# Performance work log

Measured on AMD Instinct MI355X. Metric: run time of the kernel, lower is better.

The kernel has to match this reference:

```python
import jax, jax.numpy as jnp
import numpy as np

H, HKV, D, HID = 64, 8, 64, 2880
T = 2048
WINDOW = 128
THETA = 150000.0
FACTOR = 32.0
ORIG_MAX = 4096
BETA_FAST, BETA_SLOW = 32.0, 1.0
EPS = 1e-5
SCALE = D ** -0.5
MSCALE = float(0.1 * np.log(FACTOR) + 1.0)  # vLLM YaRN attention mscale


def _yarn_inv_freq():
    # vLLM YaRNScalingRotaryEmbedding inverse frequencies
    def corr_dim(n_rot):
        return D * np.log(ORIG_MAX / (n_rot * 2.0 * np.pi)) / (2.0 * np.log(THETA))
    low = max(int(np.floor(corr_dim(BETA_FAST))), 0)
    high = min(int(np.ceil(corr_dim(BETA_SLOW))), D - 1)
    pow_ = np.arange(0, D, 2, dtype=np.float32) / D
    extrap = 1.0 / (THETA ** pow_)                 # extrapolation inv_freq
    interp = extrap / FACTOR                        # interpolation inv_freq
    ramp = np.clip((np.arange(D // 2, dtype=np.float32) - low) / max(high - low, 1e-3), 0.0, 1.0)
    extrap_mask = 1.0 - ramp
    inv_freq = interp * (1.0 - extrap_mask) + extrap * extrap_mask
    return jnp.asarray(inv_freq, jnp.float32)

_INV_FREQ = _yarn_inv_freq()


def _rope(positions, x):
    # neox-style rotation; x: [T, heads, D]
    freqs = positions.astype(jnp.float32)[:, None] * _INV_FREQ[None, :]  # [T, D/2]
    cos = (jnp.cos(freqs) * MSCALE)[:, None, :]
    sin = (jnp.sin(freqs) * MSCALE)[:, None, :]
    x1, x2 = x[..., : D // 2], x[..., D // 2 :]
    return jnp.concatenate([x1 * cos - x2 * sin, x2 * cos + x1 * sin], axis=-1)


def _attn(q, k, v, sinks):
    # q: [T,H,D]; k,v: [T,HKV,D]; sinks: [H] extra softmax logit per head
    g = H // HKV
    k = jnp.repeat(k, g, axis=1)
    v = jnp.repeat(v, g, axis=1)
    scores = jnp.einsum('qhd,khd->hqk', q, k) * SCALE  # [H,T,T]
    i = jnp.arange(T)[:, None]
    j = jnp.arange(T)[None, :]
    mask = (j <= i) & (i - j < WINDOW)  # causal + sliding window (even layer)
    scores = jnp.where(mask[None], scores, -jnp.inf)
    s = sinks[:, None]                                    # [H,1]
    m = jnp.maximum(jnp.max(scores, axis=-1), s)          # [H,T]
    p = jnp.exp(scores - m[..., None])                    # [H,T,T]
    denom = jnp.sum(p, axis=-1) + jnp.exp(s - m)          # sink adds to denominator only
    out = jnp.einsum('hqk,khd->qhd', p, v) / denom.T[..., None]
    return out.reshape(T, H * D)


def setup_inputs() -> dict:
    key = jax.random.key(0)
    ks = jax.random.split(key, 8)
    return {
        'hidden_states': jax.random.normal(ks[0], (T, HID), jnp.float32),
        'positions': jnp.arange(T, dtype=jnp.int32),
        'norm_w': jnp.ones((HID,), jnp.float32),
        'w_qkv': jax.random.normal(ks[1], ((H + 2 * HKV) * D, HID), jnp.float32) * 0.02,
        'b_qkv': jax.random.normal(ks[2], ((H + 2 * HKV) * D,), jnp.float32) * 0.02,
        'w_o': jax.random.normal(ks[3], (HID, H * D), jnp.float32) * 0.02,
        'b_o': jax.random.normal(ks[4], (HID,), jnp.float32) * 0.02,
        'sinks': jax.random.normal(ks[5], (H,), jnp.float32),
    }


def reference(hidden_states, positions, norm_w, w_qkv, b_qkv, w_o, b_o, sinks):
    x = hidden_states
    t = x * jax.lax.rsqrt(jnp.mean(x * x, axis=-1, keepdims=True) + EPS) * norm_w  # RMSNorm
    qkv = t @ w_qkv.T + b_qkv
    q, k, v = jnp.split(qkv, [H * D, H * D + HKV * D], axis=-1)
    q = _rope(positions, q.reshape(T, H, D))
    k = _rope(positions, k.reshape(T, HKV, D))
    v = v.reshape(T, HKV, D)
    attn_out = _attn(q, k, v, sinks)
    out = attn_out @ w_o.T + b_o
    return out + x  # residual
```

## Files before the change

kernel.cpp:

```cpp
#include <hip/hip_runtime.h>
#include <hip/hip_bf16.h>
#include <stdint.h>

typedef __attribute__((ext_vector_type(8))) short bf16x8;
typedef __attribute__((ext_vector_type(4))) float f32x4;
typedef __attribute__((ext_vector_type(4))) unsigned short u16x4;

#define T_SEQ 2048
#define HID_D 2880
#define KPAD 2944
#define NH 64
#define NKV 8
#define HD 64
#define QKV_N 5120
#define ATT_N 4096
#define WIN 128
#define RSCALE 0.125f
#define MSCALE 1.3465735903f
#define ROPE_TOT (T_SEQ * (NH + NKV) * 32)
#define VT_TOT (NKV * HD * T_SEQ)

__device__ __forceinline__ unsigned short f2bf(float f) {
  union { float f; unsigned u; } v; v.f = f;
  unsigned r = v.u + 0x7fffu + ((v.u >> 16) & 1u);
  return (unsigned short)(r >> 16);
}
__device__ __forceinline__ float bf2f(unsigned short u) {
  union { unsigned u; float f; } v; v.u = ((unsigned)u) << 16;
  return v.f;
}

__device__ __forceinline__ void gload_lds16(const void* g, void* l) {
  __builtin_amdgcn_global_load_lds((const __attribute__((address_space(1))) char*)g,
                                   (__attribute__((address_space(3))) char*)l, 16, 0, 0);
}

__global__ __launch_bounds__(256) void pre_kernel(const float* __restrict__ x,
                                                  const float* __restrict__ w,
                                                  unsigned short* __restrict__ t_bf,
                                                  const float* __restrict__ wq_src,
                                                  unsigned short* __restrict__ wq_dst) {
  __shared__ float red[256];
  if (blockIdx.x < 2048) {
    int row = blockIdx.x;
    const float4* xr4 = (const float4*)(x + (size_t)row * HID_D);
    const float4* w4 = (const float4*)w;
    float ss = 0.f;
    for (int i = threadIdx.x; i < 720; i += 256) {
      float4 v = xr4[i];
      ss += v.x * v.x + v.y * v.y + v.z * v.z + v.w * v.w;
    }
    red[threadIdx.x] = ss;
    __syncthreads();
    for (int s = 128; s > 0; s >>= 1) {
      if (threadIdx.x < s) red[threadIdx.x] += red[threadIdx.x + s];
      __syncthreads();
    }
    float rs = rsqrtf(red[0] / (float)HID_D + 1e-5f);
    u16x4* ob = (u16x4*)(t_bf + (size_t)row * KPAD);
    for (int i = threadIdx.x; i < 736; i += 256) {
      u16x4 o = {0, 0, 0, 0};
      if (i < 720) {
        float4 v = xr4[i];
        float4 g = w4[i];
        o = { f2bf(v.x * rs * g.x), f2bf(v.y * rs * g.y),
              f2bf(v.z * rs * g.z), f2bf(v.w * rs * g.w) };
      }
      ob[i] = o;
    }
  } else {
    const int total = QKV_N * 736;
    for (int i = (blockIdx.x - 2048) * 256 + threadIdx.x; i < total; i += 1024 * 256) {
      int c4 = i % 736, row = i / 736;
      u16x4 o = {0, 0, 0, 0};
      if (c4 < 720) {
        float4 v = ((const float4*)wq_src)[(size_t)row * 720 + c4];
        o = { f2bf(v.x), f2bf(v.y), f2bf(v.z), f2bf(v.w) };
      }
      ((u16x4*)wq_dst)[i] = o;
    }
  }
}

__device__ __forceinline__ void gemm_body(const unsigned short* __restrict__ A,
                                          const unsigned short* __restrict__ B,
                                          unsigned short* __restrict__ C,
                                          const float* __restrict__ bias,
                                          int N, int ld, int nt,
                                          int nbx, int nstore, int swz,
                                          unsigned short* sA, unsigned short* sB) {
  const int tid = threadIdx.x;
  const int lane = tid & 63, wid = tid >> 6;
  const int wr = wid >> 2, wc = wid & 3;
  const int lq = lane & 15, ro = lane >> 4;

  const int bx = swz % nbx, by = swz / nbx;
  const int m0 = by * 256, n0 = bx * 256;

  const int R0 = tid >> 3;
  const int g0 = (((tid & 7) ^ (R0 & 7)) << 3);
  const size_t aOff = (size_t)(m0 + R0) * ld + g0;
  size_t bOff[2][2];
#pragma unroll
  for (int h = 0; h < 2; ++h)
#pragma unroll
    for (int r = 0; r < 2; ++r) {
      int rr = n0 + h * 128 + r * 64 + R0;
      bOff[h][r] = (size_t)rr * ld + g0;
    }

  const int ck0 = ((ro ^ (lq & 7)) << 3);
  const int ck1 = (((4 + ro) ^ (lq & 7)) << 3);

#define STG_A(BUF, H, KT)                                                        \
  { unsigned short* _d = sA + ((BUF) * 2 + (H)) * 8192 + wid * 512;              \
    const unsigned short* _s = A + aOff + (size_t)((H) * 128) * ld + (KT) * 64;  \
    gload_lds16(_s, _d); gload_lds16(_s + (size_t)64 * ld, _d + 4096); }
#define STG_B(BUF, H, KT)                                                        \
  { unsigned short* _d = sB + ((BUF) * 2 + (H)) * 8192 + wid * 512;              \
    gload_lds16(B + bOff[H][0] + (KT) * 64, _d);                                 \
    gload_lds16(B + bOff[H][1] + (KT) * 64, _d + 4096); }

  bf16x8 aR[8];
  bf16x8 bR0[4], bR1[4];
  f32x4 acc[8][4] = {};

#define LDA(BUF, S)                                                                        \
  { _Pragma("unroll") for (int ii = 0; ii < 4; ++ii) {                                     \
      const int _r = ((BUF) * 2 + wr) * 8192 + ((S) * 64 + ii * 16 + lq) * 64;             \
      aR[ii * 2 + 0] = *(const bf16x8*)&sA[_r + ck0];                                      \
      aR[ii * 2 + 1] = *(const bf16x8*)&sA[_r + ck1]; } }
#define LDB(BUF, NHF, DST)                                                                 \
  { _Pragma("unroll") for (int jj = 0; jj < 2; ++jj) {                                     \
      const int _r = ((BUF) * 2 + (wc >> 1)) * 8192 +                                      \
                     ((wc & 1) * 64 + ((NHF) * 2 + jj) * 16 + lq) * 64;                    \
      DST[jj * 2 + 0] = *(const bf16x8*)&sB[_r + ck0];                                     \
      DST[jj * 2 + 1] = *(const bf16x8*)&sB[_r + ck1]; } }
#define MFMA16(S, NHF, BREG)                                                               \
  { _Pragma("unroll") for (int ii = 0; ii < 4; ++ii)                                       \
    _Pragma("unroll") for (int jj = 0; jj < 2; ++jj)                                       \
    _Pragma("unroll") for (int kk = 0; kk < 2; ++kk)                                       \
      acc[(S) * 4 + ii][(NHF) * 2 + jj] = __builtin_amdgcn_mfma_f32_16x16x32_bf16(         \
          aR[ii * 2 + kk], BREG[jj * 2 + kk], acc[(S) * 4 + ii][(NHF) * 2 + jj], 0, 0, 0); }
#define PH_MID()                                         \
  __builtin_amdgcn_s_barrier();                          \
  asm volatile("s_waitcnt lgkmcnt(0)" ::: "memory");     \
  __builtin_amdgcn_sched_barrier(0);                     \
  __builtin_amdgcn_s_setprio(1)
#define PH_END()                                         \
  __builtin_amdgcn_s_setprio(0);                         \
  __builtin_amdgcn_s_barrier()

  STG_A(0, 0, 0); STG_A(0, 1, 0); STG_B(0, 0, 0); STG_B(0, 1, 0);
  STG_B(1, 0, 1); STG_B(1, 1, 1);
  asm volatile("s_waitcnt vmcnt(4)" ::: "memory");
  __builtin_amdgcn_s_barrier();

  const int niter = nt >> 1;
  for (int it = 0; it < niter; ++it) {
    const int t = it * 2;
    const bool more = (it + 1 < niter);
    LDA(0, 0); LDB(0, 0, bR0); STG_A(1, 0, t + 1);
    PH_MID(); MFMA16(0, 0, bR0); PH_END();
    LDB(0, 1, bR1); STG_A(1, 1, t + 1);
    PH_MID(); MFMA16(0, 1, bR1); PH_END();
    LDA(0, 1); if (more) STG_B(0, 0, t + 2);
    PH_MID(); MFMA16(1, 1, bR1); PH_END();
    if (more) STG_B(0, 1, t + 2);
    PH_MID(); MFMA16(1, 0, bR0);
    __builtin_amdgcn_s_setprio(0);
    if (more) asm volatile("s_waitcnt vmcnt(4)" ::: "memory");
    else      asm volatile("s_waitcnt vmcnt(0)" ::: "memory");
    __builtin_amdgcn_s_barrier();
    LDA(1, 0); LDB(1, 0, bR0); if (more) STG_A(0, 0, t + 2);
    PH_MID(); MFMA16(0, 0, bR0); PH_END();
    LDB(1, 1, bR1); if (more) STG_A(0, 1, t + 2);
    PH_MID(); MFMA16(0, 1, bR1); PH_END();
    LDA(1, 1); if (more) STG_B(1, 0, t + 3);
    PH_MID(); MFMA16(1, 1, bR1); PH_END();
    if (more) STG_B(1, 1, t + 3);
    PH_MID(); MFMA16(1, 0, bR0);
    __builtin_amdgcn_s_setprio(0);
    if (more) asm volatile("s_waitcnt vmcnt(4)" ::: "memory");
    else      asm volatile("s_waitcnt vmcnt(0)" ::: "memory");
    __builtin_amdgcn_s_barrier();
  }
#undef STG_A
#undef STG_B
#undef LDA
#undef LDB
#undef MFMA16
#undef PH_MID
#undef PH_END

#pragma unroll
  for (int fi = 0; fi < 8; ++fi) {
    const int gr = m0 + wr * 128 + fi * 16 + ro * 4;
#pragma unroll
    for (int j = 0; j < 4; ++j) {
      const int gc = n0 + wc * 64 + j * 16 + lq;
      const float bv = bias[gc];
#pragma unroll
      for (int r = 0; r < 4; ++r)
        C[(size_t)(gr + r) * nstore + gc] = f2bf(acc[fi][j][r] + bv);
    }
  }
}

__global__ __launch_bounds__(512, 2) void qkv_fused_kernel(const unsigned short* __restrict__ A,
                                                           const unsigned short* __restrict__ B,
                                                           unsigned short* __restrict__ C,
                                                           const float* __restrict__ bias,
                                                           const float* __restrict__ wo_src,
                                                           unsigned short* __restrict__ wo_dst) {
  __shared__ unsigned short sA[2 * 2 * 128 * 64];
  __shared__ unsigned short sB[2 * 2 * 128 * 64];
  const int c = blockIdx.x & 7, q = blockIdx.x >> 3;
  if (q < 20) {
    const int by = (c & 1) * 4 + (q & 3);
    const int bx = (c >> 1) * 5 + (q >> 2);
    gemm_body(A, B, C, bias, QKV_N, KPAD, 46, 20, QKV_N, by * 20 + bx, sA, sB);
  } else {
    const int cid = c * 12 + (q - 20);
    const int total = HID_D * 1024;
    for (int i = cid * 512 + threadIdx.x; i < total; i += 96 * 512) {
      float4 v = ((const float4*)wo_src)[i];
      u16x4 o = { f2bf(v.x), f2bf(v.y), f2bf(v.z), f2bf(v.w) };
      ((u16x4*)wo_dst)[i] = o;
    }
  }
}

__global__ __launch_bounds__(512, 2) void outproj128_kernel(const unsigned short* __restrict__ att,
                                                            const unsigned short* __restrict__ wo,
                                                            float* __restrict__ out,
                                                            const float* __restrict__ b_o,
                                                            const float* __restrict__ x) {
  __shared__ unsigned short sA[2 * 128 * 64];
  __shared__ unsigned short sB[3 * 2 * 128 * 64];

  const int tid = threadIdx.x;
  const int lane = tid & 63, wid = tid >> 6;
  const int wr = wid >> 2, wc = wid & 3;
  const int lq = lane & 15, ro = lane >> 4;

  const int c = blockIdx.x & 7, q = blockIdx.x >> 3;
  const int by = (c & 1) * 8 + (q & 7);
  const int bx = (c >> 1) * 3 + (q >> 3);
  const int m0 = by * 128, n0 = bx * 256;

  const int R0 = tid >> 3;
  const int g0 = (((tid & 7) ^ (R0 & 7)) << 3);
  const size_t aOff = (size_t)(m0 + R0) * ATT_N + g0;
  size_t bOff[2][2];
#pragma unroll
  for (int h = 0; h < 2; ++h)
#pragma unroll
    for (int r = 0; r < 2; ++r) {
      int rr = min(n0 + h * 128 + r * 64 + R0, HID_D - 1);
      bOff[h][r] = (size_t)rr * ATT_N + g0;
    }

  const int ck0 = ((ro ^ (lq & 7)) << 3);
  const int ck1 = (((4 + ro) ^ (lq & 7)) << 3);

#define OSTG_A(BUF, KT)                                                         \
  { unsigned short* _d = sA + (BUF) * 8192 + wid * 512;                         \
    const unsigned short* _s = att + aOff + (size_t)(KT) * 64;                  \
    gload_lds16(_s, _d); gload_lds16(_s + (size_t)64 * ATT_N, _d + 4096); }
#define OSTG_B(BUF, H, KT)                                                      \
  { unsigned short* _d = sB + ((BUF) * 2 + (H)) * 8192 + wid * 512;             \
    gload_lds16(wo + bOff[H][0] + (KT) * 64, _d);                               \
    gload_lds16(wo + bOff[H][1] + (KT) * 64, _d + 4096); }

  bf16x8 aR[8];
  bf16x8 bR0[4], bR1[4];
  f32x4 acc[4][4] = {};

#define OLDA(BUF)                                                                          \
  { _Pragma("unroll") for (int ii = 0; ii < 4; ++ii) {                                     \
      const int _r = (BUF) * 8192 + (wr * 64 + ii * 16 + lq) * 64;                         \
      aR[ii * 2 + 0] = *(const bf16x8*)&sA[_r + ck0];                                      \
      aR[ii * 2 + 1] = *(const bf16x8*)&sA[_r + ck1]; } }
#define OLDB(BUF, NHF, DST)                                                                \
  { _Pragma("unroll") for (int jj = 0; jj < 2; ++jj) {                                     \
      const int _r = ((BUF) * 2 + (wc >> 1)) * 8192 +                                      \
                     ((wc & 1) * 64 + ((NHF) * 2 + jj) * 16 + lq) * 64;                    \
      DST[jj * 2 + 0] = *(const bf16x8*)&sB[_r + ck0];                                     \
      DST[jj * 2 + 1] = *(const bf16x8*)&sB[_r + ck1]; } }
#define OMFMA(NHF, BREG)                                                                   \
  { _Pragma("unroll") for (int ii = 0; ii < 4; ++ii)                                       \
    _Pragma("unroll") for (int jj = 0; jj < 2; ++jj)                                       \
    _Pragma("unroll") for (int kk = 0; kk < 2; ++kk)                                       \
      acc[ii][(NHF) * 2 + jj] = __builtin_amdgcn_mfma_f32_16x16x32_bf16(                   \
          aR[ii * 2 + kk], BREG[jj * 2 + kk], acc[ii][(NHF) * 2 + jj], 0, 0, 0); }
#define OPH_MID()                                        \
  __builtin_amdgcn_s_barrier();                          \
  asm volatile("s_waitcnt lgkmcnt(0)" ::: "memory");     \
  __builtin_amdgcn_sched_barrier(0);                     \
  __builtin_amdgcn_s_setprio(1)
#define OPH_END()                                        \
  __builtin_amdgcn_s_setprio(0);                         \
  __builtin_amdgcn_s_barrier()

  OSTG_B(0, 0, 0); OSTG_B(0, 1, 0); OSTG_A(0, 0);
  OSTG_B(1, 0, 1); OSTG_B(1, 1, 1); OSTG_A(1, 1);
  asm volatile("s_waitcnt vmcnt(6)" ::: "memory");
  __builtin_amdgcn_s_barrier();

  const int nt = 64;
  for (int it = 0; it < nt / 2; ++it) {
    const int T = it * 2;
    const bool more = (T + 2 < nt);
    const int bb0 = T % 3, bb1 = (T + 1) % 3;
    const int bb2 = (T + 2) % 3, bb3 = (T + 3) % 3;
    OLDA(T & 1); OLDB(bb0, 0, bR0);
    if (more) { OSTG_B(bb2, 0, T + 2); OSTG_B(bb2, 1, T + 2); }
    OPH_MID(); OMFMA(0, bR0); OPH_END();
    OLDB(bb0, 1, bR1);
    if (more) OSTG_A(T & 1, T + 2);
    OPH_MID(); OMFMA(1, bR1);
    __builtin_amdgcn_s_setprio(0);
    if (more) asm volatile("s_waitcnt vmcnt(6)" ::: "memory");
    else      asm volatile("s_waitcnt vmcnt(0)" ::: "memory");
    __builtin_amdgcn_s_barrier();
    OLDA((T + 1) & 1); OLDB(bb1, 0, bR0);
    if (more) { OSTG_B(bb3, 0, T + 3); OSTG_B(bb3, 1, T + 3); }
    OPH_MID(); OMFMA(0, bR0); OPH_END();
    OLDB(bb1, 1, bR1);
    if (more) OSTG_A((T + 1) & 1, T + 3);
    OPH_MID(); OMFMA(1, bR1);
    __builtin_amdgcn_s_setprio(0);
    if (more) asm volatile("s_waitcnt vmcnt(6)" ::: "memory");
    else      asm volatile("s_waitcnt vmcnt(0)" ::: "memory");
    __builtin_amdgcn_s_barrier();
  }
#undef OSTG_A
#undef OSTG_B
#undef OLDA
#undef OLDB
#undef OMFMA
#undef OPH_MID
#undef OPH_END

#pragma unroll
  for (int ii = 0; ii < 4; ++ii) {
    const int gr = m0 + wr * 64 + ii * 16 + ro * 4;
#pragma unroll
    for (int j = 0; j < 4; ++j) {
      const int gc = n0 + wc * 64 + j * 16 + lq;
      if (gc < HID_D) {
        const float bv = b_o[gc];
#pragma unroll
        for (int r = 0; r < 4; ++r) {
          size_t off = (size_t)(gr + r) * HID_D + gc;
          out[off] = acc[ii][j][r] + bv + x[off];
        }
      }
    }
  }
}

__global__ __launch_bounds__(256) void ropev_kernel(const unsigned short* __restrict__ qkvb,
                                                    const int* __restrict__ positions,
                                                    unsigned short* __restrict__ qb,
                                                    unsigned short* __restrict__ kb,
                                                    unsigned short* __restrict__ vt) {
  int idx = blockIdx.x * 256 + threadIdx.x;
  if (idx < ROPE_TOT) {
    int d = idx & 31;
    int head = (idx >> 5) % (NH + NKV);
    int t = idx / ((NH + NKV) * 32);
    float pw = (float)d * (1.0f / 32.0f);
    float extrap = expf(-pw * 11.9183905733f);
    float interp = extrap * (1.0f / 32.0f);
    float ramp = fminf(fmaxf(((float)d - 8.0f) * 0.1f, 0.0f), 1.0f);
    float invf = interp * ramp + extrap * (1.0f - ramp);
    float fr = (float)positions[t] * invf;
    float s, c;
    sincosf(fr, &s, &c);
    c *= MSCALE;
    s *= MSCALE;
    if (head < NH) {
      const unsigned short* b = qkvb + (size_t)t * QKV_N + head * HD + d;
      float x1 = bf2f(b[0]), x2 = bf2f(b[32]);
      unsigned short* ob = qb + (size_t)t * ATT_N + head * HD + d;
      ob[0] = f2bf(x1 * c - x2 * s);
      ob[32] = f2bf(x2 * c + x1 * s);
    } else {
      int gk = head - NH;
      const unsigned short* b = qkvb + (size_t)t * QKV_N + NH * HD + gk * HD + d;
      float x1 = bf2f(b[0]), x2 = bf2f(b[32]);
      unsigned short* ob = kb + (size_t)t * (NKV * HD) + gk * HD + d;
      ob[0] = f2bf(x1 * c - x2 * s);
      ob[32] = f2bf(x2 * c + x1 * s);
    }
  } else {
    int i2 = idx - ROPE_TOT;
    int t = i2 & (T_SEQ - 1);
    int d = (i2 >> 11) & 63;
    int g = i2 >> 17;
    vt[i2] = qkvb[(size_t)t * QKV_N + (NH + NKV) * HD + g * HD + d];
  }
}

__global__ __launch_bounds__(256) void attn_kernel(const unsigned short* __restrict__ qb,
                                                   const unsigned short* __restrict__ kb,
                                                   const unsigned short* __restrict__ vt,
                                                   const float* __restrict__ sinks,
                                                   unsigned short* __restrict__ att) {
  const int lane = threadIdx.x & 63;
  const int wid = threadIdx.x >> 6;
  const int q0 = blockIdx.x * 16;
  const int h = blockIdx.y * 4 + wid;
  const int g = h >> 3;
  const int lq = lane & 15;
  const int ro = lane >> 4;

  bf16x8 bq0, bq1;
  {
    const unsigned short* qp = qb + (size_t)(q0 + lq) * ATT_N + h * HD + ro * 8;
    bq0 = *(const bf16x8*)qp;
    bq1 = *(const bf16x8*)(qp + 32);
  }
  float m_run = sinks[h];
  float l_run = 1.0f;
  f32x4 o0 = {0.f, 0.f, 0.f, 0.f}, o1 = o0, o2 = o0, o3 = o0;
  const int qg = q0 + lq;
  const int jstart = (q0 >= WIN) ? q0 - WIN : 0;

  for (int jt = jstart; jt <= q0; jt += 32) {
    f32x4 st0 = {0.f, 0.f, 0.f, 0.f}, st1 = st0;
    {
      int kr = jt + ((lq >> 2) << 3) + (lq & 3);
      int kr0 = min(kr, T_SEQ - 1);
      int kr1 = min(kr + 4, T_SEQ - 1);
      const unsigned short* kp0 = kb + (size_t)kr0 * (NKV * HD) + g * HD + ro * 8;
      const unsigned short* kp1 = kb + (size_t)kr1 * (NKV * HD) + g * HD + ro * 8;
      bf16x8 ka0a = *(const bf16x8*)kp0;
      bf16x8 ka0b = *(const bf16x8*)(kp0 + 32);
      bf16x8 ka1a = *(const bf16x8*)kp1;
      bf16x8 ka1b = *(const bf16x8*)(kp1 + 32);
      st0 = __builtin_amdgcn_mfma_f32_16x16x32_bf16(ka0a, bq0, st0, 0, 0, 0);
      st0 = __builtin_amdgcn_mfma_f32_16x16x32_bf16(ka0b, bq1, st0, 0, 0, 0);
      st1 = __builtin_amdgcn_mfma_f32_16x16x32_bf16(ka1a, bq0, st1, 0, 0, 0);
      st1 = __builtin_amdgcn_mfma_f32_16x16x32_bf16(ka1b, bq1, st1, 0, 0, 0);
    }
    float p[8];
    float tmax = -3.0e30f;
#pragma unroll
    for (int r = 0; r < 4; ++r) {
      int jg0 = jt + ro * 8 + r;
      int jg1 = jg0 + 4;
      float s0 = (jg0 <= qg && (qg - jg0) < WIN) ? st0[r] * RSCALE : -3.0e30f;
      float s1 = (jg1 <= qg && (qg - jg1) < WIN) ? st1[r] * RSCALE : -3.0e30f;
      p[r] = s0;
      p[r + 4] = s1;
      tmax = fmaxf(tmax, fmaxf(s0, s1));
    }
    tmax = fmaxf(tmax, __shfl_xor(tmax, 16));
    tmax = fmaxf(tmax, __shfl_xor(tmax, 32));
    float m_new = fmaxf(m_run, tmax);
    float rescale = expf(m_run - m_new);
    float psum = 0.f;
    bf16x8 pa;
#pragma unroll
    for (int jj = 0; jj < 8; ++jj) {
      float pe = expf(p[jj] - m_new);
      psum += pe;
      pa[jj] = (short)f2bf(pe);
    }
    psum += __shfl_xor(psum, 16);
    psum += __shfl_xor(psum, 32);
    l_run = l_run * rescale + psum;
    m_run = m_new;
    f32x4 rs4;
#pragma unroll
    for (int r = 0; r < 4; ++r) rs4[r] = __shfl(rescale, ro * 4 + r);
    o0 *= rs4; o1 *= rs4; o2 *= rs4; o3 *= rs4;
    int tb = jt + ro * 8;
    if (tb > T_SEQ - 8) tb = T_SEQ - 8;
    const unsigned short* vp = vt + (size_t)(g * HD + lq) * T_SEQ + tb;
    bf16x8 v0 = *(const bf16x8*)vp;
    bf16x8 v1 = *(const bf16x8*)(vp + 16 * T_SEQ);
    bf16x8 v2 = *(const bf16x8*)(vp + 32 * T_SEQ);
    bf16x8 v3 = *(const bf16x8*)(vp + 48 * T_SEQ);
    o0 = __builtin_amdgcn_mfma_f32_16x16x32_bf16(pa, v0, o0, 0, 0, 0);
    o1 = __builtin_amdgcn_mfma_f32_16x16x32_bf16(pa, v1, o1, 0, 0, 0);
    o2 = __builtin_amdgcn_mfma_f32_16x16x32_bf16(pa, v2, o2, 0, 0, 0);
    o3 = __builtin_amdgcn_mfma_f32_16x16x32_bf16(pa, v3, o3, 0, 0, 0);
  }

#pragma unroll
  for (int r = 0; r < 4; ++r) {
    float lr = __shfl(l_run, ro * 4 + r);
    float inv = 1.0f / lr;
    int qrow = q0 + ro * 4 + r;
    unsigned short* op = att + (size_t)qrow * ATT_N + h * HD + lq;
    op[0] = f2bf(o0[r] * inv);
    op[16] = f2bf(o1[r] * inv);
    op[32] = f2bf(o2[r] * inv);
    op[48] = f2bf(o3[r] * inv);
  }
}

extern "C" void kernel_launch(void* const* d_in, const int* in_sizes, int n_in,
                              void* d_out, int out_size, void* d_ws, size_t ws_size,
                              hipStream_t stream) {
  const float* x = (const float*)d_in[0];
  const int* pos = (const int*)d_in[1];
  const float* norm_w = (const float*)d_in[2];
  const float* w_qkv = (const float*)d_in[3];
  const float* b_qkv = (const float*)d_in[4];
  const float* w_o = (const float*)d_in[5];
  const float* b_o = (const float*)d_in[6];
  const float* sinks = (const float*)d_in[7];
  float* out = (float*)d_out;

  unsigned short* t_bf = (unsigned short*)d_ws;
  unsigned short* wq_bf = t_bf + (size_t)T_SEQ * KPAD;
  unsigned short* wo_bf = wq_bf + (size_t)QKV_N * KPAD;
  unsigned short* qkv_bf = wo_bf + (size_t)HID_D * ATT_N;
  unsigned short* qb = qkv_bf + (size_t)T_SEQ * QKV_N;
  unsigned short* kb = qb + (size_t)T_SEQ * ATT_N;
  unsigned short* vt = kb + (size_t)T_SEQ * NKV * HD;
  unsigned short* att = vt + (size_t)NKV * HD * T_SEQ;

  pre_kernel<<<3072, 256, 0, stream>>>(x, norm_w, t_bf, w_qkv, wq_bf);
  qkv_fused_kernel<<<256, 512, 0, stream>>>(t_bf, wq_bf, qkv_bf, b_qkv, w_o, wo_bf);
  ropev_kernel<<<(ROPE_TOT + VT_TOT) / 256, 256, 0, stream>>>(qkv_bf, pos, qb, kb, vt);
  attn_kernel<<<dim3(T_SEQ / 16, NH / 4), 256, 0, stream>>>(qb, kb, vt, sinks, att);
  outproj128_kernel<<<192, 512, 0, stream>>>(att, wo_bf, out, b_o, x);
}
```

Measured before the change: 249.9 us.

## Tile V transpose via LDS, coalesce attention stores, zero-pad Wo rows

Moves the V transpose out of the rope kernel into a dedicated LDS-tiled kernel that reads and writes 16-byte vectors. Attention output is staged through shared memory so each wave writes full 128-byte rows instead of scattered 2-byte stores. The bf16 Wo copy is padded to 3072 rows with zeros, which removes the row clamping in the out-projection loads. Costs are an extra kernel launch, some extra shared memory in the attention kernel, and a larger workspace.

```diff
diff --git a/kernel.cpp b/kernel.cpp
--- a/kernel.cpp
+++ b/kernel.cpp
@@ -3,6 +3,7 @@
 #include <stdint.h>
 
 typedef __attribute__((ext_vector_type(8))) short bf16x8;
+typedef __attribute__((ext_vector_type(8))) unsigned short u16x8;
 typedef __attribute__((ext_vector_type(4))) float f32x4;
 typedef __attribute__((ext_vector_type(4))) unsigned short u16x4;
 
@@ -14,11 +15,11 @@
 #define HD 64
 #define QKV_N 5120
 #define ATT_N 4096
+#define NOPAD 3072
 #define WIN 128
 #define RSCALE 0.125f
 #define MSCALE 1.3465735903f
 #define ROPE_TOT (T_SEQ * (NH + NKV) * 32)
-#define VT_TOT (NKV * HD * T_SEQ)
 
 __device__ __forceinline__ unsigned short f2bf(float f) {
   union { float f; unsigned u; } v; v.f = f;
@@ -222,10 +223,13 @@
     gemm_body(A, B, C, bias, QKV_N, KPAD, 46, 20, QKV_N, by * 20 + bx, sA, sB);
   } else {
     const int cid = c * 12 + (q - 20);
-    const int total = HID_D * 1024;
+    const int total = NOPAD * 1024;
     for (int i = cid * 512 + threadIdx.x; i < total; i += 96 * 512) {
-      float4 v = ((const float4*)wo_src)[i];
-      u16x4 o = { f2bf(v.x), f2bf(v.y), f2bf(v.z), f2bf(v.w) };
+      u16x4 o = {0, 0, 0, 0};
+      if (i < HID_D * 1024) {
+        float4 v = ((const float4*)wo_src)[i];
+        o = { f2bf(v.x), f2bf(v.y), f2bf(v.z), f2bf(v.w) };
+      }
       ((u16x4*)wo_dst)[i] = o;
     }
   }
@@ -257,7 +261,7 @@
   for (int h = 0; h < 2; ++h)
 #pragma unroll
     for (int r = 0; r < 2; ++r) {
-      int rr = min(n0 + h * 128 + r * 64 + R0, HID_D - 1);
+      int rr = n0 + h * 128 + r * 64 + R0;
       bOff[h][r] = (size_t)rr * ATT_N + g0;
     }
 
@@ -364,44 +368,60 @@
 __global__ __launch_bounds__(256) void ropev_kernel(const unsigned short* __restrict__ qkvb,
                                                     const int* __restrict__ positions,
                                                     unsigned short* __restrict__ qb,
-                                                    unsigned short* __restrict__ kb,
-                                                    unsigned short* __restrict__ vt) {
+                                                    unsigned short* __restrict__ kb) {
   int idx = blockIdx.x * 256 + threadIdx.x;
-  if (idx < ROPE_TOT) {
-    int d = idx & 31;
-    int head = (idx >> 5) % (NH + NKV);
-    int t = idx / ((NH + NKV) * 32);
-    float pw = (float)d * (1.0f / 32.0f);
-    float extrap = expf(-pw * 11.9183905733f);
-    float interp = extrap * (1.0f / 32.0f);
-    float ramp = fminf(fmaxf(((float)d - 8.0f) * 0.1f, 0.0f), 1.0f);
-    float invf = interp * ramp + extrap * (1.0f - ramp);
-    float fr = (float)positions[t] * invf;
-    float s, c;
-    sincosf(fr, &s, &c);
-    c *= MSCALE;
-    s *= MSCALE;
-    if (head < NH) {
-      const unsigned short* b = qkvb + (size_t)t * QKV_N + head * HD + d;
-      float x1 = bf2f(b[0]), x2 = bf2f(b[32]);
-      unsigned short* ob = qb + (size_t)t * ATT_N + head * HD + d;
-      ob[0] = f2bf(x1 * c - x2 * s);
-      ob[32] = f2bf(x2 * c + x1 * s);
-    } else {
-      int gk = head - NH;
-      const unsigned short* b = qkvb + (size_t)t * QKV_N + NH * HD + gk * HD + d;
-      float x1 = bf2f(b[0]), x2 = bf2f(b[32]);
-      unsigned short* ob = kb + (size_t)t * (NKV * HD) + gk * HD + d;
-      ob[0] = f2bf(x1 * c - x2 * s);
-      ob[32] = f2bf(x2 * c + x1 * s);
-    }
+  int d = idx & 31;
+  int head = (idx >> 5) % (NH + NKV);
+  int t = idx / ((NH + NKV) * 32);
+  float pw = (float)d * (1.0f / 32.0f);
+  float extrap = expf(-pw * 11.9183905733f);
+  float interp = extrap * (1.0f / 32.0f);
+  float ramp = fminf(fmaxf(((float)d - 8.0f) * 0.1f, 0.0f), 1.0f);
+  float invf = interp * ramp + extrap * (1.0f - ramp);
+  float fr = (float)positions[t] * invf;
+  float s, c;
+  sincosf(fr, &s, &c);
+  c *= MSCALE;
+  s *= MSCALE;
+  if (head < NH) {
+    const unsigned short* b = qkvb + (size_t)t * QKV_N + head * HD + d;
+    float x1 = bf2f(b[0]), x2 = bf2f(b[32]);
+    unsigned short* ob = qb + (size_t)t * ATT_N + head * HD + d;
+    ob[0] = f2bf(x1 * c - x2 * s);
+    ob[32] = f2bf(x2 * c + x1 * s);
   } else {
-    int i2 = idx - ROPE_TOT;
-    int t = i2 & (T_SEQ - 1);
-    int d = (i2 >> 11) & 63;
-    int g = i2 >> 17;
-    vt[i2] = qkvb[(size_t)t * QKV_N + (NH + NKV) * HD + g * HD + d];
-  }
+    int gk = head - NH;
+    const unsigned short* b = qkvb + (size_t)t * QKV_N + NH * HD + gk * HD + d;
+    float x1 = bf2f(b[0]), x2 = bf2f(b[32]);
+    unsigned short* ob = kb + (size_t)t * (NKV * HD) + gk * HD + d;
+    ob[0] = f2bf(x1 * c - x2 * s);
+    ob[32] = f2bf(x2 * c + x1 * s);
+  }
+}
+
+__global__ __launch_bounds__(256) void vtrans_kernel(const unsigned short* __restrict__ qkvb,
+                                                     unsigned short* __restrict__ vt) {
+  __shared__ unsigned short tile[64][72];
+  const int g = blockIdx.x >> 5;
+  const int t0 = (blockIdx.x & 31) << 6;
+  const int r = threadIdx.x >> 3;
+  const int c8 = (threadIdx.x & 7) << 3;
+  const size_t vbase = (size_t)(NH + NKV) * HD + (size_t)g * HD;
+#pragma unroll
+  for (int hh = 0; hh < 2; ++hh) {
+    int row = r + hh * 32;
+    *(u16x8*)&tile[row][c8] =
+        *(const u16x8*)(qkvb + (size_t)(t0 + row) * QKV_N + vbase + c8);
+  }
+  __syncthreads();
+  const int d = threadIdx.x >> 2;
+  const int ts = (threadIdx.x & 3) << 4;
+  u16x8 v0, v1;
+#pragma unroll
+  for (int i = 0; i < 8; ++i) { v0[i] = tile[ts + i][d]; v1[i] = tile[ts + 8 + i][d]; }
+  unsigned short* dst = vt + (size_t)(g * HD + d) * T_SEQ + t0 + ts;
+  *(u16x8*)dst = v0;
+  *(u16x8*)(dst + 8) = v1;
 }
 
 __global__ __launch_bounds__(256) void attn_kernel(const unsigned short* __restrict__ qb,
@@ -409,6 +429,7 @@
                                                    const unsigned short* __restrict__ vt,
                                                    const float* __restrict__ sinks,
                                                    unsigned short* __restrict__ att) {
+  __shared__ unsigned short orep[4][16][72];
   const int lane = threadIdx.x & 63;
   const int wid = threadIdx.x >> 6;
   const int q0 = blockIdx.x * 16;
@@ -495,12 +516,20 @@
   for (int r = 0; r < 4; ++r) {
     float lr = __shfl(l_run, ro * 4 + r);
     float inv = 1.0f / lr;
-    int qrow = q0 + ro * 4 + r;
-    unsigned short* op = att + (size_t)qrow * ATT_N + h * HD + lq;
-    op[0] = f2bf(o0[r] * inv);
-    op[16] = f2bf(o1[r] * inv);
-    op[32] = f2bf(o2[r] * inv);
-    op[48] = f2bf(o3[r] * inv);
+    int row = ro * 4 + r;
+    orep[wid][row][lq]      = f2bf(o0[r] * inv);
+    orep[wid][row][lq + 16] = f2bf(o1[r] * inv);
+    orep[wid][row][lq + 32] = f2bf(o2[r] * inv);
+    orep[wid][row][lq + 48] = f2bf(o3[r] * inv);
+  }
+  {
+    const int row = lane >> 2;
+    const int seg = (lane & 3) << 4;
+    u16x8 w0 = *(const u16x8*)&orep[wid][row][seg];
+    u16x8 w1 = *(const u16x8*)&orep[wid][row][seg + 8];
+    unsigned short* op = att + (size_t)(q0 + row) * ATT_N + h * HD + seg;
+    *(u16x8*)op = w0;
+    *(u16x8*)(op + 8) = w1;
   }
 }
 
@@ -520,7 +549,7 @@
   unsigned short* t_bf = (unsigned short*)d_ws;
   unsigned short* wq_bf = t_bf + (size_t)T_SEQ * KPAD;
   unsigned short* wo_bf = wq_bf + (size_t)QKV_N * KPAD;
-  unsigned short* qkv_bf = wo_bf + (size_t)HID_D * ATT_N;
+  unsigned short* qkv_bf = wo_bf + (size_t)NOPAD * ATT_N;
   unsigned short* qb = qkv_bf + (size_t)T_SEQ * QKV_N;
   unsigned short* kb = qb + (size_t)T_SEQ * ATT_N;
   unsigned short* vt = kb + (size_t)T_SEQ * NKV * HD;
@@ -528,7 +557,8 @@
 
   pre_kernel<<<3072, 256, 0, stream>>>(x, norm_w, t_bf, w_qkv, wq_bf);
   qkv_fused_kernel<<<256, 512, 0, stream>>>(t_bf, wq_bf, qkv_bf, b_qkv, w_o, wo_bf);
-  ropev_kernel<<<(ROPE_TOT + VT_TOT) / 256, 256, 0, stream>>>(qkv_bf, pos, qb, kb, vt);
+  ropev_kernel<<<ROPE_TOT / 256, 256, 0, stream>>>(qkv_bf, pos, qb, kb);
+  vtrans_kernel<<<256, 256, 0, stream>>>(qkv_bf, vt);
   attn_kernel<<<dim3(T_SEQ / 16, NH / 4), 256, 0, stream>>>(qb, kb, vt, sinks, att);
   outproj128_kernel<<<192, 512, 0, stream>>>(att, wo_bf, out, b_o, x);
 }
```

After: 250.2 us. About the same (+0.1%).
